# Kernel optimization log

Hardware: AMD Instinct MI355X
Metric: run time of the kernel (lower is better)

## Reference

```python
import jax, jax.numpy as jnp
import numpy as np

SIGMA = 2.5
EPS = 0.01


def cdist(a, b):
    # a: [n,3], b: [m,3] -> [n,m] euclidean distances (|a|^2 + |b|^2 - 2 a.b trick)
    d2 = (jnp.sum(a * a, axis=-1)[:, None]
          + jnp.sum(b * b, axis=-1)[None, :]
          - 2.0 * a @ b.T)
    return jnp.sqrt(jnp.maximum(d2, 0.0))


def torch_rbf(points_1, points_2, feats_1, sigma=SIGMA, eps=EPS):
    # points_1: [n,3] source, points_2: [m,3] targets, feats_1: [n,k] -> [m,k+1]
    all_dists = cdist(points_2, points_1)                # [m,n]
    rbf_w = jnp.exp(-all_dists / sigma)
    line_norms = jnp.sum(rbf_w, axis=1) + eps            # [m]
    rbf_w = rbf_w / line_norms[:, None]
    feats_2 = rbf_w @ feats_1                            # [m,k]
    return jnp.concatenate([feats_2, jnp.tanh(line_norms)[:, None]], axis=1)


def setup_inputs() -> dict:
    key = jax.random.key(0)
    ks = jax.random.split(key, 12)
    L, N, Dg = 4096, 40000, 12
    inp = {
        "locs_left": jax.random.normal(ks[0], (L, 3), jnp.float32),
        "locs_right": jax.random.normal(ks[1], (L, 3), jnp.float32),
        "g1_pos": jax.random.normal(ks[2], (N, 3), jnp.float32),
        "g1_x": jax.random.normal(ks[3], (N, Dg), jnp.float32),
        "g2_pos": jax.random.normal(ks[4], (N, 3), jnp.float32),
        "g2_x": jax.random.normal(ks[5], (N, Dg), jnp.float32),
        "s1_verts": jax.random.normal(ks[6], (N, 3), jnp.float32),
        "s1_x": jax.random.normal(ks[7], (N, Dg), jnp.float32),
        "s2_verts": jax.random.normal(ks[8], (N, 3), jnp.float32),
        "s2_x": jax.random.normal(ks[9], (N, Dg), jnp.float32),
        "W1": jax.random.normal(ks[10], (50, 50), jnp.float32) * 0.1,
        "b1": jnp.zeros((50,), jnp.float32),
        "W2": jax.random.normal(ks[11], (50, 1), jnp.float32) * 0.1,
        "b2": jnp.zeros((1,), jnp.float32),
    }
    return inp


def reference(locs_left, locs_right, g1_pos, g1_x, g2_pos, g2_x,
              s1_verts, s1_x, s2_verts, s2_x, W1, b1, W2, b2):
    # nearest graph node gather (argmin over node dim)
    idx_l = jnp.argmin(cdist(locs_left, g1_pos), axis=1)     # [L]
    processed_left = g1_x[idx_l]                              # [L,12]
    idx_r = jnp.argmin(cdist(locs_right, g2_pos), axis=1)
    processed_right = g2_x[idx_r]                             # [L,12]

    feats_left = torch_rbf(s1_verts, locs_left, s1_x)         # [L,13]
    feats_right = torch_rbf(s2_verts, locs_right, s2_x)       # [L,13]

    x = jnp.concatenate([processed_left, feats_left,
                         processed_right, feats_right], axis=1)  # [L,50]
    h = jax.nn.relu(x @ W1 + b1)   # dropout is identity at eval
    return h @ W2 + b2             # [L,1]
```

## Files before the change

kernel.cpp:

```cpp
#include <hip/hip_runtime.h>
#include <hip/hip_bf16.h>
#include <cstdint>
#include <cstddef>

#define BLK 256
#define DG 12

static constexpr float EPS_ = 0.01f;
static constexpr float C2SQ_     = 0.333019070232236f;
static constexpr float TWO_C2SQ_ = 0.666038140464472f;

typedef __attribute__((ext_vector_type(2))) float v2f;
typedef __attribute__((ext_vector_type(8))) short v8s;
typedef __attribute__((ext_vector_type(4))) float v4f;

__device__ __forceinline__ void gl16(const void* g, void* l) {
    __builtin_amdgcn_global_load_lds(
        (const __attribute__((address_space(1))) void*)g,
        (__attribute__((address_space(3))) void*)l,
        16, 0, 0);
}

__global__ __launch_bounds__(BLK) void pip_pack(
    const float* __restrict__ g1_pos, const float* __restrict__ g2_pos,
    const float* __restrict__ s1_v,   const float* __restrict__ s1_x,
    const float* __restrict__ s2_v,   const float* __restrict__ s2_x,
    float4* __restrict__ pk1s, int4* __restrict__ fpk,
    float* __restrict__ red, unsigned long long* __restrict__ keys,
    int N, int T, int L)
{
#pragma clang fp contract(off)
    const int P = T * 16;
    const int tid = blockIdx.x * BLK + threadIdx.x;

    if (tid < 26 * L) red[tid] = 0.f;
    else if (tid < 28 * L) keys[tid - 26 * L] = ~0ull;

    if (tid < 2 * P) {
        const int side = tid / P;
        const int pr = tid - side * P;
        const float* src = side ? g2_pos : g1_pos;
        const int n0 = 2 * pr, n1 = 2 * pr + 1;
        float x0 = 1e9f, y0 = 1e9f, z0 = 1e9f, h0 = 1.5e18f;
        float x1 = 1e9f, y1 = 1e9f, z1 = 1e9f, h1 = 1.5e18f;
        if (n0 < N) {
            x0 = src[3 * n0]; y0 = src[3 * n0 + 1]; z0 = src[3 * n0 + 2];
            h0 = 0.5f * ((x0 * x0 + y0 * y0) + z0 * z0);
        }
        if (n1 < N) {
            x1 = src[3 * n1]; y1 = src[3 * n1 + 1]; z1 = src[3 * n1 + 2];
            h1 = 0.5f * ((x1 * x1 + y1 * y1) + z1 * z1);
        }
        pk1s[(size_t)tid * 2 + 0] = make_float4(x0, x1, y0, y1);
        pk1s[(size_t)tid * 2 + 1] = make_float4(z0, z1, h0, h1);
    } else {
        const int u = tid - 2 * P;
        if (u < 128 * T) {
            const int side = u / (64 * T);
            const int r = u - side * 64 * T;
            const int t = r >> 6;
            const int ln = r & 63;
            const float* X = side ? s2_x : s1_x;
            const int nb = 32 * t + ((ln >> 4) << 3);
            const int feat = ln & 15;
            int w[4];
#pragma unroll
            for (int d = 0; d < 4; ++d) {
                const int n0 = nb + 2 * d, n1 = nb + 2 * d + 1;
                const float f0 = (n0 < N) ? (feat < 12 ? X[(size_t)n0 * DG + feat] : (feat == 12 ? 1.f : 0.f)) : 0.f;
                const float f1 = (n1 < N) ? (feat < 12 ? X[(size_t)n1 * DG + feat] : (feat == 12 ? 1.f : 0.f)) : 0.f;
                __hip_bfloat162 h = __float22bfloat162_rn(make_float2(f0, f1));
                __builtin_memcpy(&w[d], &h, 4);
            }
            fpk[((size_t)side * T + t) * 64 + ln] = make_int4(w[0], w[1], w[2], w[3]);
        }
    }
}

__global__ __launch_bounds__(256, 4) void pip_partial(
    const float* __restrict__ locs_l, const float* __restrict__ locs_r,
    const float4* __restrict__ pk1s, const int4* __restrict__ fpk,
    float* __restrict__ red, unsigned long long* __restrict__ keys,
    int L, int T, int CT, int P)
{
#pragma clang fp contract(off)
    const int lane = threadIdx.x & 63;
    const int wv = threadIdx.x >> 6;
    const int g = lane >> 4;
    const int side = blockIdx.z;
    const int qbase = blockIdx.x * 128 + wv * 32;

    const float* __restrict__ locs = side ? locs_r : locs_l;

    float qxm[2], qym[2], qzm[2], nqhm[2];
#pragma unroll
    for (int mt = 0; mt < 2; ++mt) {
        const int qm = qbase + 16 * mt + (lane & 15);
        const float a = locs[3 * qm + 0];
        const float b = locs[3 * qm + 1];
        const float c = locs[3 * qm + 2];
        qxm[mt] = a; qym[mt] = b; qzm[mt] = c;
        nqhm[mt] = 0.5f * ((a * a + b * b) + c * c);
    }

    v4f cC[2];
#pragma unroll
    for (int mt = 0; mt < 2; ++mt) cC[mt] = (v4f)0.f;

    float rbd[2];
    int rtl[2];
    const int t0 = blockIdx.y * CT;
#pragma unroll
    for (int mt = 0; mt < 2; ++mt) { rbd[mt] = 3.4e38f; rtl[mt] = t0; }

    __shared__ __align__(16) unsigned char smem[2][3072];

    const int t1 = (t0 + CT < T) ? (t0 + CT) : T;
    const int np = (t1 - t0) >> 1;

    const unsigned char* gpk = (const unsigned char*)pk1s
        + ((size_t)side * P + (size_t)t0 * 16) * 32 + (size_t)lane * 16;
    const unsigned char* gfp = (const unsigned char*)fpk
        + ((size_t)side * T + t0) * 1024 + (size_t)lane * 16;

    if (wv == 0) gl16(gpk, &smem[0][0]);
    else if (wv == 1) gl16(gfp, &smem[0][1024]);
    else if (wv == 2) gl16(gfp + 1024, &smem[0][2048]);
    __syncthreads();

#pragma unroll 1
    for (int pp = 0; pp < np; ++pp) {
        unsigned char* const cbuf = &smem[pp & 1][0];
        if (pp + 1 < np) {
            unsigned char* const nbuf = &smem[(pp & 1) ^ 1][0];
            const size_t o1 = (size_t)(pp + 1) * 1024;
            const size_t o2 = (size_t)(pp + 1) * 2048;
            if (wv == 0) gl16(gpk + o1, nbuf);
            else if (wv == 1) gl16(gfp + o2, nbuf + 1024);
            else if (wv == 2) gl16(gfp + o2 + 1024, nbuf + 2048);
        }

#pragma unroll
        for (int tp = 0; tp < 2; ++tp) {
            const int tg = t0 + 2 * pp + tp;
            const v8s b = *(const v8s*)(cbuf + 1024 + tp * 1024 + lane * 16);
            union AF { int i[4]; v8s s; };
            AF af[2];
            const unsigned char* pbase = cbuf + tp * 512 + (4 * g) * 32;

            v2f tvm[2];
#pragma unroll
            for (int dp = 0; dp < 4; ++dp) {
                const float4 XY = *(const float4*)(pbase + dp * 32);
                const float4 ZH = *(const float4*)(pbase + dp * 32 + 16);
                const v2f xx = {XY.x, XY.y}, yy = {XY.z, XY.w};
                const v2f zz = {ZH.x, ZH.y}, hh = {ZH.z, ZH.w};

#pragma unroll
                for (int mt = 0; mt < 2; ++mt) {
                    const v2f qx2 = {qxm[mt], qxm[mt]};
                    const v2f qy2 = {qym[mt], qym[mt]};
                    const v2f qz2 = {qzm[mt], qzm[mt]};
                    const v2f S = nqhm[mt] + hh;
                    v2f d2 = __builtin_elementwise_fma(-qx2, xx, S);
                    d2 = __builtin_elementwise_fma(-qy2, yy, d2);
                    d2 = __builtin_elementwise_fma(-qz2, zz, d2);

                    tvm[mt] = (dp == 0) ? d2 : __builtin_elementwise_min(tvm[mt], d2);

                    const v2f t = d2 * TWO_C2SQ_;
                    const float w0 = __builtin_amdgcn_exp2f(-__builtin_amdgcn_sqrtf(__builtin_fabsf(t.x)));
                    const float w1 = __builtin_amdgcn_exp2f(-__builtin_amdgcn_sqrtf(__builtin_fabsf(t.y)));
                    int pk;
                    asm("v_cvt_pk_bf16_f32 %0, %1, %2" : "=v"(pk) : "v"(w0), "v"(w1));
                    af[mt].i[dp] = pk;
                }
            }

#pragma unroll
            for (int mt = 0; mt < 2; ++mt) {
                const float m = fminf(tvm[mt].x, tvm[mt].y);
                const bool c = m < rbd[mt];
                rbd[mt] = c ? m : rbd[mt];
                rtl[mt] = c ? tg : rtl[mt];
            }

#pragma unroll
            for (int mt = 0; mt < 2; ++mt)
                cC[mt] = __builtin_amdgcn_mfma_f32_16x16x32_bf16(af[mt].s, b, cC[mt], 0, 0, 0);
        }

        __syncthreads();
    }

    const int feat = lane & 15;
    if (feat < 13) {
        const int slot = side * 13 + feat;
#pragma unroll
        for (int mt = 0; mt < 2; ++mt)
#pragma unroll
            for (int r = 0; r < 4; ++r) {
                const int q = qbase + 16 * mt + ((lane >> 4) << 2) + r;
                atomicAdd(&red[(size_t)slot * L + q], cC[mt][r]);
            }
    }

    const float4* __restrict__ pk1b = pk1s + (size_t)side * P * 2;
    unsigned idxm[2];
#pragma unroll
    for (int mt = 0; mt < 2; ++mt) {
        const int tw = rtl[mt];
        const float4* wp = pk1b + ((size_t)tw * 16 + 4 * g) * 2;
        unsigned idx = 0u;
#pragma unroll
        for (int dp = 3; dp >= 0; --dp) {
            const float4 XY = wp[2 * dp + 0];
            const float4 ZH = wp[2 * dp + 1];
            const float S0 = nqhm[mt] + ZH.z;
            const float d0 = __builtin_fmaf(-qzm[mt], ZH.x,
                               __builtin_fmaf(-qym[mt], XY.z,
                                 __builtin_fmaf(-qxm[mt], XY.x, S0)));
            const float S1 = nqhm[mt] + ZH.w;
            const float d1 = __builtin_fmaf(-qzm[mt], ZH.y,
                               __builtin_fmaf(-qym[mt], XY.w,
                                 __builtin_fmaf(-qxm[mt], XY.y, S1)));
            const unsigned base = 2u * (unsigned)(tw * 16 + 4 * g + dp);
            if (d1 == rbd[mt]) idx = base | 1u;
            if (d0 == rbd[mt]) idx = base;
        }
        idxm[mt] = idx;
    }

    unsigned long long km[2];
#pragma unroll
    for (int mt = 0; mt < 2; ++mt)
        km[mt] = ((unsigned long long)__float_as_uint(rbd[mt]) << 32)
               | (unsigned long long)idxm[mt];
#pragma unroll
    for (int mt = 0; mt < 2; ++mt) {
#pragma unroll
        for (int m = 16; m <= 32; m <<= 1) {
            const unsigned lo = (unsigned)km[mt];
            const unsigned hi = (unsigned)(km[mt] >> 32);
            const unsigned lo2 = __shfl_xor(lo, m, 64);
            const unsigned hi2 = __shfl_xor(hi, m, 64);
            const unsigned long long o = ((unsigned long long)hi2 << 32)
                                       | (unsigned long long)lo2;
            km[mt] = (o < km[mt]) ? o : km[mt];
        }
    }
    if (lane < 32) {
        const unsigned long long kk = (lane & 16) ? km[1] : km[0];
        atomicMin(&keys[(size_t)side * L + qbase + lane], kk);
    }
}

__device__ __forceinline__ float tanh_pos(float x) {
    const float t = __expf(-2.f * x);
    return (1.f - t) / (1.f + t);
}

__global__ __launch_bounds__(BLK) void pip_final(
    const float* __restrict__ red, const unsigned long long* __restrict__ keys,
    const float* __restrict__ g1_x, const float* __restrict__ g2_x,
    const float* __restrict__ W1, const float* __restrict__ b1,
    const float* __restrict__ W2, const float* __restrict__ b2,
    float* __restrict__ out, int L)
{
#pragma clang fp contract(off)
    const int l = blockIdx.x * BLK + threadIdx.x;
    if (l >= L) return;

    const unsigned idxL = (unsigned)(keys[l] & 0xffffffffull);
    const unsigned idxR = (unsigned)(keys[(size_t)L + l] & 0xffffffffull);
    const float normL = red[(size_t)12 * L + (size_t)l] + EPS_;
    const float normR = red[(size_t)25 * L + (size_t)l] + EPS_;

    float x[50];
    {
        const float4* f = (const float4*)(g1_x + (size_t)idxL * DG);
        const float4 f0 = f[0], f1 = f[1], f2 = f[2];
        x[0] = f0.x; x[1] = f0.y; x[2]  = f0.z; x[3]  = f0.w;
        x[4] = f1.x; x[5] = f1.y; x[6]  = f1.z; x[7]  = f1.w;
        x[8] = f2.x; x[9] = f2.y; x[10] = f2.z; x[11] = f2.w;
    }
#pragma unroll
    for (int k = 0; k < DG; ++k) x[12 + k] = red[(size_t)k * L + (size_t)l] / normL;
    x[24] = tanh_pos(normL);
    {
        const float4* f = (const float4*)(g2_x + (size_t)idxR * DG);
        const float4 f0 = f[0], f1 = f[1], f2 = f[2];
        x[25] = f0.x; x[26] = f0.y; x[27] = f0.z; x[28] = f0.w;
        x[29] = f1.x; x[30] = f1.y; x[31] = f1.z; x[32] = f1.w;
        x[33] = f2.x; x[34] = f2.y; x[35] = f2.z; x[36] = f2.w;
    }
#pragma unroll
    for (int k = 0; k < DG; ++k) x[37 + k] = red[(size_t)(13 + k) * L + (size_t)l] / normR;
    x[49] = tanh_pos(normR);

    float h[50];
#pragma unroll
    for (int j = 0; j < 50; ++j) h[j] = b1[j];
#pragma unroll
    for (int k = 0; k < 50; ++k) {
        const float xk = x[k];
#pragma unroll
        for (int j = 0; j < 50; ++j) h[j] = fmaf(xk, W1[k * 50 + j], h[j]);
    }
    float o = b2[0];
#pragma unroll
    for (int j = 0; j < 50; ++j) o = fmaf(fmaxf(h[j], 0.f), W2[j], o);
    out[l] = o;
}

extern "C" void kernel_launch(void* const* d_in, const int* in_sizes, int n_in,
                              void* d_out, int out_size, void* d_ws, size_t ws_size,
                              hipStream_t stream) {
    const float* locs_l = (const float*)d_in[0];
    const float* locs_r = (const float*)d_in[1];
    const float* g1_pos = (const float*)d_in[2];
    const float* g1_x   = (const float*)d_in[3];
    const float* g2_pos = (const float*)d_in[4];
    const float* g2_x   = (const float*)d_in[5];
    const float* s1_v   = (const float*)d_in[6];
    const float* s1_x   = (const float*)d_in[7];
    const float* s2_v   = (const float*)d_in[8];
    const float* s2_x   = (const float*)d_in[9];
    const float* W1     = (const float*)d_in[10];
    const float* b1     = (const float*)d_in[11];
    const float* W2     = (const float*)d_in[12];
    const float* b2     = (const float*)d_in[13];
    float* out = (float*)d_out;
    float* ws  = (float*)d_ws;

    const int L = in_sizes[0] / 3;
    const int N = in_sizes[2] / 3;
    const int T = (N + 31) / 32;
    const int P = T * 16;

    const size_t o_fpk = (size_t)256 * T;
    const size_t o_red = (size_t)768 * T;

    const int CT = 20;
    const int SC = (T + CT - 1) / CT;

    float4* pk1s = (float4*)ws;
    int4*   fpk  = (int4*)(ws + o_fpk);
    float*  red  = ws + o_red;
    unsigned long long* keys = (unsigned long long*)(red + (size_t)26 * L);

    const int ptasks = 160 * T;
    pip_pack<<<dim3((ptasks + BLK - 1) / BLK), dim3(BLK), 0, stream>>>(
        g1_pos, g2_pos, s1_v, s1_x, s2_v, s2_x, pk1s, fpk, red, keys, N, T, L);

    pip_partial<<<dim3(L / 128, SC, 2), dim3(256), 0, stream>>>(
        locs_l, locs_r, pk1s, fpk, red, keys, L, T, CT, P);

    pip_final<<<dim3((L + BLK - 1) / BLK), dim3(BLK), 0, stream>>>(
        red, keys, g1_x, g2_x, W1, b1, W2, b2, out, L);
}
```

Measured before the change: 243.4 us.

## Give each wave private LDS double buffers and load B fragments into registers

Replaces the block-shared LDS double buffer, where three waves each staged a slice, with per-wave private LDS buffers for the point-pack data. The MFMA B-operand fragments are now loaded straight into registers from global memory. Block-wide __syncthreads barriers are swapped for manual s_waitcnt vmcnt counting in a two-stage unrolled loop. The goal is to remove barrier stalls and let each wave prefetch on its own. The cost is that every wave now loads the shared point data redundantly, and correctness rests on the hand-set vmcnt values and on the compiler not reordering the loads.

After: 241.7 us. No clear change (-0.7%).

```diff
diff --git a/kernel.cpp b/kernel.cpp
--- a/kernel.cpp
+++ b/kernel.cpp
@@ -113,37 +113,29 @@
 #pragma unroll
     for (int mt = 0; mt < 2; ++mt) { rbd[mt] = 3.4e38f; rtl[mt] = t0; }
 
-    __shared__ __align__(16) unsigned char smem[2][3072];
+    __shared__ __align__(16) unsigned char smem[4][2][1024];
+    unsigned char* const buf0 = &smem[wv][0][0];
+    unsigned char* const buf1 = &smem[wv][1][0];
 
     const int t1 = (t0 + CT < T) ? (t0 + CT) : T;
     const int np = (t1 - t0) >> 1;
 
     const unsigned char* gpk = (const unsigned char*)pk1s
         + ((size_t)side * P + (size_t)t0 * 16) * 32 + (size_t)lane * 16;
-    const unsigned char* gfp = (const unsigned char*)fpk
-        + ((size_t)side * T + t0) * 1024 + (size_t)lane * 16;
-
-    if (wv == 0) gl16(gpk, &smem[0][0]);
-    else if (wv == 1) gl16(gfp, &smem[0][1024]);
-    else if (wv == 2) gl16(gfp + 1024, &smem[0][2048]);
-    __syncthreads();
-
-#pragma unroll 1
-    for (int pp = 0; pp < np; ++pp) {
-        unsigned char* const cbuf = &smem[pp & 1][0];
-        if (pp + 1 < np) {
-            unsigned char* const nbuf = &smem[(pp & 1) ^ 1][0];
-            const size_t o1 = (size_t)(pp + 1) * 1024;
-            const size_t o2 = (size_t)(pp + 1) * 2048;
-            if (wv == 0) gl16(gpk + o1, nbuf);
-            else if (wv == 1) gl16(gfp + o2, nbuf + 1024);
-            else if (wv == 2) gl16(gfp + o2 + 1024, nbuf + 2048);
-        }
-
+    const v8s* __restrict__ gfb = (const v8s*)fpk
+        + ((size_t)side * T + t0) * 64 + lane;
+
+    gl16(gpk, buf0);
+    v8s b0A = gfb[0];
+    v8s b0B = gfb[64];
+    v8s b1A, b1B;
+
+    auto COMPUTE = [&](const unsigned char* cbuf, const v8s& bA_, const v8s& bB_,
+                       const int tgb) {
 #pragma unroll
         for (int tp = 0; tp < 2; ++tp) {
-            const int tg = t0 + 2 * pp + tp;
-            const v8s b = *(const v8s*)(cbuf + 1024 + tp * 1024 + lane * 16);
+            const int tg = tgb + tp;
+            const v8s b = tp ? bB_ : bA_;
             union AF { int i[4]; v8s s; };
             AF af[2];
             const unsigned char* pbase = cbuf + tp * 512 + (4 * g) * 32;
@@ -189,8 +181,32 @@
             for (int mt = 0; mt < 2; ++mt)
                 cC[mt] = __builtin_amdgcn_mfma_f32_16x16x32_bf16(af[mt].s, b, cC[mt], 0, 0, 0);
         }
-
-        __syncthreads();
+    };
+
+    int pp = 0;
+    while (pp < np) {
+        if (pp + 1 < np) {
+            gl16(gpk + (size_t)(pp + 1) * 1024, buf1);
+            b1A = gfb[(size_t)(2 * pp + 2) * 64];
+            b1B = gfb[(size_t)(2 * pp + 3) * 64];
+            asm volatile("s_waitcnt vmcnt(3)" ::: "memory");
+        } else {
+            asm volatile("s_waitcnt vmcnt(0)" ::: "memory");
+        }
+        COMPUTE(buf0, b0A, b0B, t0 + 2 * pp);
+        ++pp;
+        if (pp >= np) break;
+
+        if (pp + 1 < np) {
+            gl16(gpk + (size_t)(pp + 1) * 1024, buf0);
+            b0A = gfb[(size_t)(2 * pp + 2) * 64];
+            b0B = gfb[(size_t)(2 * pp + 3) * 64];
+            asm volatile("s_waitcnt vmcnt(3)" ::: "memory");
+        } else {
+            asm volatile("s_waitcnt vmcnt(0)" ::: "memory");
+        }
+        COMPUTE(buf1, b1A, b1B, t0 + 2 * pp);
+        ++pp;
     }
 
     const int feat = lane & 15;
```
